# Optimization experiments

Hardware: AMD Instinct MI355X
Metric: run time of the kernel (lower is better)

Reference implementation:

```python
import jax, jax.numpy as jnp
import numpy as np

GROUPSIZE = 4      # g: multivariate group size (d = groupsize - 2)
NB_GROUPS = 48     # f: number of expert groups / filters
CHANNELS = 128     # c: signal channels fed to the L operator
SCALE = 0.999
SLOPE = 1.0        # model_params['scaling']
LAMB_INIT = 0.1
EPS_OMEGA_INIT = -2.0


def proj_l1(x):
    """Euclidean projection onto the unit l1 ball along axis 1. x: [B,G,F,H,W]."""
    ax = jnp.abs(x)
    s = -jnp.sort(-ax, axis=1)                      # descending |x|
    cssv = jnp.cumsum(s, axis=1) - 1.0
    G = x.shape[1]
    k = jnp.arange(1, G + 1, dtype=x.dtype).reshape(1, G, 1, 1, 1)
    cond = s * k > cssv
    rho = jnp.sum(cond, axis=1, keepdims=True)       # number of active coords
    theta = jnp.take_along_axis(cssv, rho - 1, axis=1) / rho.astype(x.dtype)
    theta = jnp.maximum(theta, 0.0)
    proj = jnp.sign(x) * jnp.maximum(ax - theta, 0.0)
    inside = jnp.sum(ax, axis=1, keepdims=True) <= 1.0
    return jnp.where(inside, x, proj)


def _forward(x_noisy, sigma, Q_param, taus_param, lamb, eps_omega,
             mu_w1, mu_b1, mu_w2, mu_b2, mu_w3, mu_b3, Wf, n_iter):
    lamb_e = jnp.exp(lamb)
    eps_e = jnp.exp(eps_omega)

    # --- Q normalization + spectral norms (cached once per forward) ---
    Q = Q_param / jnp.maximum(jnp.sum(jnp.abs(Q_param), axis=2, keepdims=True), 1.0)
    Q_norms = jnp.linalg.svd(Q, compute_uv=False)[:, 0].reshape(-1, 1, 1)  # [F,1,1]
    Q_eff = Q / Q_norms ** 2
    taus = jnp.exp(jax.nn.relu(taus_param))          # [1,1,F,1,1]

    # --- per-batch noise-adaptive scaling via small MLP ---
    h = jax.nn.relu((sigma * 20.0 - 2.0) @ mu_w1 + mu_b1)
    h = jax.nn.relu(h @ mu_w2 + mu_b2)
    h = h @ mu_w3 + mu_b3                            # [B,F]
    scaling = jax.nn.relu(h * 0.05 + sigma) * SLOPE + 1e-9
    scaling = scaling.reshape(-1, 1, scaling.shape[-1], 1, 1)  # [B,1,F,1,1]

    def moreau(x):
        g = proj_l1(x)
        cost = jnp.max(jnp.abs(x - g), axis=1) + 0.5 * jnp.sum(g * g, axis=1)
        cost = cost[:, None]                         # [B,1,F,H,W]
        g = g + eps_e * x
        cost = cost + eps_e * 0.5 * jnp.sqrt(jnp.sum(x * x, axis=1, keepdims=True))
        return g, cost

    def activation(x):
        gc, cc = moreau(x)
        # orient: scale * einsum('flg,bgfhw->blfhw', Q/Q_norms^2, x), then /taus
        y = SCALE * jnp.einsum('flg,bgfhw->blfhw', Q_eff, x) / taus
        gcc, ccc = moreau(y)
        # unorient: scale * einsum with Q^T  (Q^T[f,l,g] = Q[f,g,l])
        gcc = SCALE * jnp.einsum('fgl,bgfhw->blfhw', Q, gcc)
        ccc = Q_norms ** 2 * (taus * ccc)
        return lamb_e * (gc - gcc), lamb_e * (cc - ccc)

    def reconstruct(x):
        Lx = jnp.einsum('gfc,bchw->bgfhw', Wf, x) / scaling
        g, cost = activation(Lx)
        g = jnp.einsum('gfc,bgfhw->bchw', Wf, g * scaling)   # adjoint L^T
        cost = jnp.sum(cost * scaling ** 2, axis=(1, 2, 3, 4))
        g = (x - x_noisy + g) / (1.0 + lamb_e * (1.0 + eps_e))
        cost = cost + 0.5 * jnp.sum((x - x_noisy) ** 2, axis=(1, 2, 3))
        return g, cost

    def step(x, _):
        g, _c = reconstruct(x)
        return x - g, None

    x_final, _ = jax.lax.scan(jax.checkpoint(step), x_noisy, jnp.arange(n_iter))
    return x_final


def setup_inputs() -> dict:
    key = jax.random.key(0)
    ks = jax.random.split(key, 8)
    B, C, H, W = 2, CHANNELS, 128, 128
    F_, G = NB_GROUPS, GROUPSIZE
    x_noisy = jax.random.normal(ks[0], (B, C, H, W), jnp.float32)
    sigma = jax.random.uniform(ks[1], (B, 1), jnp.float32)
    Q_param = jax.random.uniform(ks[2], (F_, G, G), jnp.float32) - 0.5
    taus_param = (LAMB_INIT / 2.0) * jnp.ones((1, 1, F_, 1, 1), jnp.float32)
    lamb = jnp.float32(LAMB_INIT)
    eps_omega = jnp.float32(EPS_OMEGA_INIT)
    mu_w1 = jax.random.normal(ks[3], (1, F_), jnp.float32)
    mu_b1 = jnp.zeros((F_,), jnp.float32)
    mu_w2 = jax.random.normal(ks[4], (F_, F_), jnp.float32) / np.float32(np.sqrt(F_))
    mu_b2 = jnp.zeros((F_,), jnp.float32)
    mu_w3 = jax.random.normal(ks[5], (F_, F_), jnp.float32) / np.float32(np.sqrt(F_))
    mu_b3 = jnp.zeros((F_,), jnp.float32)
    Wf = jax.random.normal(ks[6], (G, F_, C), jnp.float32) / np.float32(np.sqrt(C))
    return dict(x_noisy=x_noisy, sigma=sigma, Q_param=Q_param, taus_param=taus_param,
                lamb=lamb, eps_omega=eps_omega, mu_w1=mu_w1, mu_b1=mu_b1,
                mu_w2=mu_w2, mu_b2=mu_b2, mu_w3=mu_w3, mu_b3=mu_b3, Wf=Wf, n_iter=10)


def reference(x_noisy, sigma, Q_param, taus_param, lamb, eps_omega,
              mu_w1, mu_b1, mu_w2, mu_b2, mu_w3, mu_b3, Wf, n_iter):
    return _forward(x_noisy, sigma, Q_param, taus_param, lamb, eps_omega,
                    mu_w1, mu_b1, mu_w2, mu_b2, mu_w3, mu_b3, Wf, n_iter)
```

## Files before the change

### kernel.cpp

```cpp
#include <hip/hip_runtime.h>
#include <math.h>

#define F_ 48
#define C_ 128
#define HW 16384
#define SCALE_C 0.999f
#define TPB 256
#define MTPB 512

typedef __attribute__((ext_vector_type(4))) float floatx4;
typedef __attribute__((ext_vector_type(8))) _Float16 half8;
typedef __attribute__((ext_vector_type(4))) _Float16 half4;

#define P1_U 0
#define P2_U 49152
#define QEQN_F 49152
#define MISC_F (QEQN_F + 1536)
#define SINV_F (MISC_F + 2)
#define SLAM_F (SINV_F + 96)

__global__ void setup_math(const float* __restrict__ sigma,
                           const float* __restrict__ Qp,
                           const float* __restrict__ taus_p,
                           const float* __restrict__ lamb,
                           const float* __restrict__ eps_om,
                           const float* __restrict__ mw1, const float* __restrict__ mb1,
                           const float* __restrict__ mw2, const float* __restrict__ mb2,
                           const float* __restrict__ mw3, const float* __restrict__ mb3,
                           float* __restrict__ wsf)
{
    const int tid = threadIdx.x;
    if (tid < F_) {
        const int f = tid;
        float Qm[4][4];
        for (int g = 0; g < 4; ++g) {
            float s = 0.f;
            for (int l = 0; l < 4; ++l) s += fabsf(Qp[f * 16 + g * 4 + l]);
            float d = fmaxf(s, 1.0f);
            for (int l = 0; l < 4; ++l) Qm[g][l] = Qp[f * 16 + g * 4 + l] / d;
        }
        double A[4][4];
        for (int i = 0; i < 4; ++i)
            for (int j = 0; j < 4; ++j) {
                double s = 0.0;
                for (int g = 0; g < 4; ++g) s += (double)Qm[g][i] * (double)Qm[g][j];
                A[i][j] = s;
            }
        double M[4][4];
        for (int i = 0; i < 4; ++i) for (int j = 0; j < 4; ++j) M[i][j] = A[i][j];
        for (int it = 0; it < 30; ++it) {
            double T[4][4]; double mx = 0.0;
            for (int i = 0; i < 4; ++i)
                for (int j = 0; j < 4; ++j) {
                    double s = 0.0;
                    for (int k = 0; k < 4; ++k) s += M[i][k] * M[k][j];
                    T[i][j] = s;
                    double a = fabs(s); if (a > mx) mx = a;
                }
            if (mx < 1e-300) break;
            double inv = 1.0 / mx;
            for (int i = 0; i < 4; ++i) for (int j = 0; j < 4; ++j) M[i][j] = T[i][j] * inv;
        }
        int jb = 0; double bn = -1.0;
        for (int j = 0; j < 4; ++j) {
            double nn = 0.0;
            for (int i = 0; i < 4; ++i) nn += M[i][j] * M[i][j];
            if (nn > bn) { bn = nn; jb = j; }
        }
        double v[4]; for (int i = 0; i < 4; ++i) v[i] = M[i][jb];
        double Av[4];
        for (int i = 0; i < 4; ++i) {
            double s = 0.0;
            for (int j = 0; j < 4; ++j) s += A[i][j] * v[j];
            Av[i] = s;
        }
        double vv = 0.0, vav = 0.0;
        for (int i = 0; i < 4; ++i) { vv += v[i] * v[i]; vav += v[i] * Av[i]; }
        float lamf = (float)((vv > 0.0) ? (vav / vv) : 0.0);
        float tau = expf(fmaxf(taus_p[f], 0.0f));
        float qsv = SCALE_C / tau;
        for (int l = 0; l < 4; ++l)
            for (int g = 0; g < 4; ++g)
                wsf[QEQN_F + f * 32 + l * 4 + g] = qsv * Qm[l][g] / lamf;
        for (int g = 0; g < 4; ++g)
            for (int l = 0; l < 4; ++l)
                wsf[QEQN_F + f * 32 + 16 + g * 4 + l] = SCALE_C * Qm[g][l];
    }
    if (tid >= 48 && tid < 50) {
        const int b = tid - 48;
        float lamb_e = expf(lamb[0]);
        float sg = sigma[b];
        float t = sg * 20.0f - 2.0f;
        float h1[F_], h2[F_];
        for (int j = 0; j < F_; ++j) h1[j] = fmaxf(t * mw1[j] + mb1[j], 0.0f);
        for (int j = 0; j < F_; ++j) {
            float s = mb2[j];
            for (int k = 0; k < F_; ++k) s += h1[k] * mw2[k * F_ + j];
            h2[j] = fmaxf(s, 0.0f);
        }
        for (int j = 0; j < F_; ++j) {
            float s = mb3[j];
            for (int k = 0; k < F_; ++k) s += h2[k] * mw3[k * F_ + j];
            float sc = fmaxf(s * 0.05f + sg, 0.0f) + 1e-9f;
            wsf[SINV_F + b * F_ + j] = 1.0f / sc;
            wsf[SLAM_F + b * F_ + j] = lamb_e * sc;
        }
    }
    if (tid == 50) {
        float lamb_e = expf(lamb[0]);
        float eps_e = expf(eps_om[0]);
        wsf[MISC_F + 0] = eps_e;
        wsf[MISC_F + 1] = 1.0f / (1.0f + lamb_e * (1.0f + eps_e));
    }
}

__global__ void setup_pack(const float* __restrict__ Wf, float* __restrict__ wsf)
{
    unsigned short* wsu = (unsigned short*)wsf;
    const int gtid = blockIdx.x * TPB + threadIdx.x;
    for (int i = gtid; i < 98304; i += gridDim.x * TPB) {
        if (i < 49152) {
            int j = i & 7, lane = (i >> 3) & 63;
            int t = i >> 9;
            int ks = t & 3, mtile = t >> 2;
            int rt = lane & 15, qq = lane >> 4;
            int c = ks * 32 + qq * 8 + j;
            int ft = mtile >> 1;
            int f = ft * 4 + (rt >> 2);
            int gl = rt & 3;
            float w;
            if ((mtile & 1) == 0) {
                w = Wf[(gl * F_ + f) * C_ + c];
            } else {
                w = 0.f;
                for (int g = 0; g < 4; ++g)
                    w += wsf[QEQN_F + f * 32 + gl * 4 + g] * Wf[(g * F_ + f) * C_ + c];
            }
            _Float16 hv = (_Float16)w;
            wsu[P1_U + ((mtile * 4 + ks) * 64 + lane) * 8 + j] = *(unsigned short*)&hv;
        } else {
            int ii = i - 49152;
            int j = ii & 7, lane = (ii >> 3) & 63;
            int t = ii >> 9;
            int ks = t % 12, cmt = t / 12;
            int m = lane & 15, qq = lane >> 4;
            int cch = cmt * 16 + m;
            int r = ks * 32 + qq * 8 + j;
            float w;
            if (ks < 6) {
                int f = r >> 2, g = r & 3;
                w = Wf[(g * F_ + f) * C_ + cch];
            } else {
                int rp = r - 192;
                int f = rp >> 2, l = rp & 3;
                w = 0.f;
                for (int g = 0; g < 4; ++g)
                    w += wsf[QEQN_F + f * 32 + 16 + l * 4 + g] * Wf[(g * F_ + f) * C_ + cch];
                w = -w;
            }
            _Float16 hv = (_Float16)w;
            wsu[P2_U + ((cmt * 12 + ks) * 64 + lane) * 8 + j] = *(unsigned short*)&hv;
        }
    }
}

__device__ __forceinline__ void proj4(const float v[4], float o[4]) {
    float a0 = fabsf(v[0]), a1 = fabsf(v[1]), a2 = fabsf(v[2]), a3 = fabsf(v[3]);
    float sum = a0 + a1 + a2 + a3;
    float t0 = fmaxf(a0, a1), u0 = fminf(a0, a1);
    float t1 = fmaxf(a2, a3), u1 = fminf(a2, a3);
    float s0 = fmaxf(t0, t1), m0 = fminf(t0, t1);
    float m1 = fmaxf(u0, u1), s3 = fminf(u0, u1);
    float s1 = fmaxf(m1, m0), s2 = fminf(m1, m0);
    float c2 = s0 + s1, c3 = c2 + s2, c4 = c3 + s3;
    float th = s0 - 1.0f, rs = 1.0f;
    if (s1 * 2.0f > c2 - 1.0f) { th = c2 - 1.0f; rs = 0.5f; }
    if (s2 * 3.0f > c3 - 1.0f) { th = c3 - 1.0f; rs = (1.0f / 3.0f); }
    if (s3 * 4.0f > c4 - 1.0f) { th = c4 - 1.0f; rs = 0.25f; }
    float theta = fmaxf(th * rs, 0.0f);
    bool inside = (sum <= 1.0f);
#pragma unroll
    for (int g = 0; g < 4; ++g) {
        float ag = fabsf(v[g]);
        float pg = copysignf(fmaxf(ag - theta, 0.0f), v[g]);
        o[g] = inside ? v[g] : pg;
    }
}

__global__ __launch_bounds__(MTPB, 4) void mfoe_main(
    const float* __restrict__ xnoisy,
    const float* __restrict__ wsf,
    float* __restrict__ out,
    const int* __restrict__ n_iter_p)
{
    __shared__ __align__(16) _Float16 sXF[4096];
    __shared__ __align__(16) _Float16 sACT[12288];
    __shared__ __align__(16) float sISL[96];

    const int tid = threadIdx.x;
    const int lane = tid & 63;
    const int wv = __builtin_amdgcn_readfirstlane(tid >> 6);
    const int n = lane & 15;
    const int q = lane >> 4;
    const int blk = blockIdx.x;
    const int b = blk >> 9;
    const int pix0 = (blk & 511) << 5;

    const float* __restrict__ xin = xnoisy + b * (C_ * HW) + pix0;
    float* __restrict__ oimg = out + b * (C_ * HW) + pix0;
    const unsigned short* __restrict__ wsu = (const unsigned short*)wsf;
    const int niter = *n_iter_p;

    if (niter == 0) {
        for (int i = tid; i < C_ * 32; i += MTPB) {
            int p = i & 31, c = i >> 5;
            oimg[c * HW + p] = xin[c * HW + p];
        }
        return;
    }

    for (int i = tid; i < C_ * 32; i += MTPB) {
        int p = i & 31, c = i >> 5;
        int idx = ((p >> 4) * 4 + (c >> 5)) * 512 + (((c >> 3) & 3) * 16 + (p & 15)) * 8 + (c & 7);
        sXF[idx] = (_Float16)xin[c * HW + p];
    }
    for (int i = tid; i < 96; i += MTPB) {
        if (i < 48) sISL[i] = wsf[SINV_F + b * F_ + i];
        else        sISL[i] = wsf[SLAM_F + b * F_ + (i - 48)];
    }

    float xnr[8];
#pragma unroll
    for (int j = 0; j < 2; ++j) {
        int jw = wv * 2 + j, cmt = jw >> 1, nt = jw & 1;
        int p = nt * 16 + n;
#pragma unroll
        for (int reg = 0; reg < 4; ++reg)
            xnr[j * 4 + reg] = xin[(cmt * 16 + q * 4 + reg) * HW + p];
    }
    const float eps_e = wsf[MISC_F + 0];
    const float invden = wsf[MISC_F + 1];

    for (int it = 0; it < niter; ++it) {
        __syncthreads();
#pragma unroll 1
        for (int j = 0; j < 3; ++j) {
            int jw = wv * 3 + j, ft = jw >> 1, nt = jw & 1;
            floatx4 accv = (floatx4){0.f, 0.f, 0.f, 0.f};
            floatx4 accy = (floatx4){0.f, 0.f, 0.f, 0.f};
            const half8* aE = (const half8*)(wsu + P1_U + (ft * 8) * 512 + lane * 8);
            const half8* bFp = (const half8*)&sXF[nt * 2048 + lane * 8];
#pragma unroll
            for (int ks = 0; ks < 4; ++ks) {
                half8 bF = bFp[ks * 64];
                accv = __builtin_amdgcn_mfma_f32_16x16x32_f16(aE[ks * 64], bF, accv, 0, 0, 0);
                accy = __builtin_amdgcn_mfma_f32_16x16x32_f16(aE[ks * 64 + 256], bF, accy, 0, 0, 0);
            }
            int f = ft * 4 + q;
            float invs = sISL[f];
            float slam = sISL[48 + f];
            float v[4] = {accv[0] * invs, accv[1] * invs, accv[2] * invs, accv[3] * invs};
            float y[4] = {accy[0] * invs, accy[1] * invs, accy[2] * invs, accy[3] * invs};
            float pv[4]; proj4(v, pv);
            float py[4]; proj4(y, py);
            half4 au, am;
#pragma unroll
            for (int g = 0; g < 4; ++g) {
                au[g] = (_Float16)(fmaf(eps_e, v[g], pv[g]) * slam);
                am[g] = (_Float16)(fmaf(eps_e, y[g], py[g]) * slam);
            }
            int aw = ((nt * 12 + (ft >> 1)) * 64 + ((ft & 1) * 2 + (q >> 1)) * 16 + n) * 8 + (q & 1) * 4;
            *(half4*)&sACT[aw] = au;
            *(half4*)&sACT[aw + 3072] = am;
        }
        __syncthreads();
        floatx4 acc2[2];
#pragma unroll
        for (int j = 0; j < 2; ++j) acc2[j] = (floatx4){0.f, 0.f, 0.f, 0.f};
#pragma unroll
        for (int j = 0; j < 2; ++j) {
            int jw = wv * 2 + j, cmt = jw >> 1, nt = jw & 1;
            const half8* a2F = (const half8*)(wsu + P2_U + (cmt * 12) * 512 + lane * 8);
            const half8* bAp = (const half8*)&sACT[nt * 6144 + lane * 8];
            floatx4 a = acc2[j];
#pragma unroll
            for (int ks = 0; ks < 12; ++ks) {
                half8 aF = a2F[ks * 64];
                half8 bA = bAp[ks * 64];
                a = __builtin_amdgcn_mfma_f32_16x16x32_f16(aF, bA, a, 0, 0, 0);
            }
            acc2[j] = a;
        }
        const bool last = (it == niter - 1);
#pragma unroll
        for (int j = 0; j < 2; ++j) {
            int jw = wv * 2 + j, cmt = jw >> 1, nt = jw & 1;
            int p = nt * 16 + n;
            int cb = cmt * 16 + q * 4;
            int xu = ((nt * 4 + (cmt >> 1)) * 64 + ((cmt & 1) * 2 + (q >> 1)) * 16 + n) * 8 + (q & 1) * 4;
            half4 xo4 = *(const half4*)&sXF[xu];
            float xo0 = (float)xo4[0];
            float xo1 = (float)xo4[1];
            float xo2 = (float)xo4[2];
            float xo3 = (float)xo4[3];
            float nx0 = xo0 - ((xo0 - xnr[j * 4 + 0]) + acc2[j][0]) * invden;
            float nx1 = xo1 - ((xo1 - xnr[j * 4 + 1]) + acc2[j][1]) * invden;
            float nx2 = xo2 - ((xo2 - xnr[j * 4 + 2]) + acc2[j][2]) * invden;
            float nx3 = xo3 - ((xo3 - xnr[j * 4 + 3]) + acc2[j][3]) * invden;
            if (last) {
                oimg[(cb + 0) * HW + p] = nx0;
                oimg[(cb + 1) * HW + p] = nx1;
                oimg[(cb + 2) * HW + p] = nx2;
                oimg[(cb + 3) * HW + p] = nx3;
            }
            half4 nx4;
            nx4[0] = (_Float16)nx0;
            nx4[1] = (_Float16)nx1;
            nx4[2] = (_Float16)nx2;
            nx4[3] = (_Float16)nx3;
            *(half4*)&sXF[xu] = nx4;
        }
    }
}

extern "C" void kernel_launch(void* const* d_in, const int* in_sizes, int n_in,
                              void* d_out, int out_size, void* d_ws, size_t ws_size,
                              hipStream_t stream) {
    const float* x_noisy = (const float*)d_in[0];
    const float* sigma   = (const float*)d_in[1];
    const float* Qp      = (const float*)d_in[2];
    const float* taus_p  = (const float*)d_in[3];
    const float* lamb    = (const float*)d_in[4];
    const float* eps_om  = (const float*)d_in[5];
    const float* mw1     = (const float*)d_in[6];
    const float* mb1     = (const float*)d_in[7];
    const float* mw2     = (const float*)d_in[8];
    const float* mb2     = (const float*)d_in[9];
    const float* mw3     = (const float*)d_in[10];
    const float* mb3     = (const float*)d_in[11];
    const float* Wf      = (const float*)d_in[12];
    const int*   n_iter  = (const int*)d_in[13];
    float* out = (float*)d_out;
    float* ws  = (float*)d_ws;

    hipLaunchKernelGGL(setup_math, dim3(1), dim3(64), 0, stream,
                       sigma, Qp, taus_p, lamb, eps_om,
                       mw1, mb1, mw2, mb2, mw3, mb3, ws);
    hipLaunchKernelGGL(setup_pack, dim3(192), dim3(TPB), 0, stream, Wf, ws);
    hipLaunchKernelGGL(mfoe_main, dim3(1024), dim3(MTPB), 0, stream,
                       x_noisy, ws, out, n_iter);
}
```

Before: 287.0 us.

## Double pixel tile per block to reuse weight fragments across four pixel tiles

Each block now handles 64 pixels instead of 32, halving the grid to 512 blocks. Each wave loads an A weight fragment once and reuses it across two pixel tiles in the first GEMM and four in the second, cutting global/L2 weight reads per MFMA. The iterate x is also kept in fp32 registers instead of being re-read from fp16 LDS, which improves precision and removes LDS reads. The cost is double LDS use, higher register pressure, and fewer blocks, which may reduce occupancy or leave CUs underfilled.

Result: no change. 283.7 us (-1.1%).

```diff
diff --git a/kernel.cpp b/kernel.cpp
--- a/kernel.cpp
+++ b/kernel.cpp
@@ -193,8 +193,8 @@
     float* __restrict__ out,
     const int* __restrict__ n_iter_p)
 {
-    __shared__ __align__(16) _Float16 sXF[4096];
-    __shared__ __align__(16) _Float16 sACT[12288];
+    __shared__ __align__(16) _Float16 sXF[8192];
+    __shared__ __align__(16) _Float16 sACT[24576];
     __shared__ __align__(16) float sISL[96];
 
     const int tid = threadIdx.x;
@@ -203,8 +203,8 @@
     const int n = lane & 15;
     const int q = lane >> 4;
     const int blk = blockIdx.x;
-    const int b = blk >> 9;
-    const int pix0 = (blk & 511) << 5;
+    const int b = blk >> 8;
+    const int pix0 = (blk & 255) << 6;
 
     const float* __restrict__ xin = xnoisy + b * (C_ * HW) + pix0;
     float* __restrict__ oimg = out + b * (C_ * HW) + pix0;
@@ -212,16 +212,16 @@
     const int niter = *n_iter_p;
 
     if (niter == 0) {
-        for (int i = tid; i < C_ * 32; i += MTPB) {
-            int p = i & 31, c = i >> 5;
+        for (int i = tid; i < C_ * 64; i += MTPB) {
+            int p = i & 63, c = i >> 6;
             oimg[c * HW + p] = xin[c * HW + p];
         }
         return;
     }
 
-    for (int i = tid; i < C_ * 32; i += MTPB) {
-        int p = i & 31, c = i >> 5;
-        int idx = ((p >> 4) * 4 + (c >> 5)) * 512 + (((c >> 3) & 3) * 16 + (p & 15)) * 8 + (c & 7);
+    for (int i = tid; i < C_ * 64; i += MTPB) {
+        int p = i & 63, c = i >> 6;
+        int idx = (((p >> 4) * 4 + (c >> 5)) * 64 + ((c >> 3) & 3) * 16 + (p & 15)) * 8 + (c & 7);
         sXF[idx] = (_Float16)xin[c * HW + p];
     }
     for (int i = tid; i < 96; i += MTPB) {
@@ -229,95 +229,96 @@
         else        sISL[i] = wsf[SLAM_F + b * F_ + (i - 48)];
     }
 
-    float xnr[8];
-#pragma unroll
-    for (int j = 0; j < 2; ++j) {
-        int jw = wv * 2 + j, cmt = jw >> 1, nt = jw & 1;
-        int p = nt * 16 + n;
-#pragma unroll
-        for (int reg = 0; reg < 4; ++reg)
-            xnr[j * 4 + reg] = xin[(cmt * 16 + q * 4 + reg) * HW + p];
-    }
+    float xnr[16], xr[16];
+#pragma unroll
+    for (int np = 0; np < 4; ++np)
+#pragma unroll
+        for (int l = 0; l < 4; ++l) {
+            float v = xin[(wv * 16 + q * 4 + l) * HW + np * 16 + n];
+            xnr[np * 4 + l] = v;
+            xr[np * 4 + l] = v;
+        }
     const float eps_e = wsf[MISC_F + 0];
     const float invden = wsf[MISC_F + 1];
 
     for (int it = 0; it < niter; ++it) {
         __syncthreads();
 #pragma unroll 1
-        for (int j = 0; j < 3; ++j) {
-            int jw = wv * 3 + j, ft = jw >> 1, nt = jw & 1;
-            floatx4 accv = (floatx4){0.f, 0.f, 0.f, 0.f};
-            floatx4 accy = (floatx4){0.f, 0.f, 0.f, 0.f};
+        for (int jj = 0; jj < 3; ++jj) {
+            int grp = wv * 3 + jj, ft = grp >> 1, nph = grp & 1;
+            int np0 = nph * 2;
+            floatx4 accv0 = (floatx4){0.f, 0.f, 0.f, 0.f};
+            floatx4 accv1 = (floatx4){0.f, 0.f, 0.f, 0.f};
+            floatx4 accy0 = (floatx4){0.f, 0.f, 0.f, 0.f};
+            floatx4 accy1 = (floatx4){0.f, 0.f, 0.f, 0.f};
             const half8* aE = (const half8*)(wsu + P1_U + (ft * 8) * 512 + lane * 8);
-            const half8* bFp = (const half8*)&sXF[nt * 2048 + lane * 8];
+            const half8* b0 = (const half8*)&sXF[(np0 * 4) * 512 + lane * 8];
+            const half8* b1 = (const half8*)&sXF[((np0 + 1) * 4) * 512 + lane * 8];
 #pragma unroll
             for (int ks = 0; ks < 4; ++ks) {
-                half8 bF = bFp[ks * 64];
-                accv = __builtin_amdgcn_mfma_f32_16x16x32_f16(aE[ks * 64], bF, accv, 0, 0, 0);
-                accy = __builtin_amdgcn_mfma_f32_16x16x32_f16(aE[ks * 64 + 256], bF, accy, 0, 0, 0);
+                half8 aV = aE[ks * 64];
+                half8 aY = aE[ks * 64 + 256];
+                half8 bF0 = b0[ks * 64];
+                half8 bF1 = b1[ks * 64];
+                accv0 = __builtin_amdgcn_mfma_f32_16x16x32_f16(aV, bF0, accv0, 0, 0, 0);
+                accy0 = __builtin_amdgcn_mfma_f32_16x16x32_f16(aY, bF0, accy0, 0, 0, 0);
+                accv1 = __builtin_amdgcn_mfma_f32_16x16x32_f16(aV, bF1, accv1, 0, 0, 0);
+                accy1 = __builtin_amdgcn_mfma_f32_16x16x32_f16(aY, bF1, accy1, 0, 0, 0);
             }
             int f = ft * 4 + q;
             float invs = sISL[f];
             float slam = sISL[48 + f];
-            float v[4] = {accv[0] * invs, accv[1] * invs, accv[2] * invs, accv[3] * invs};
-            float y[4] = {accy[0] * invs, accy[1] * invs, accy[2] * invs, accy[3] * invs};
-            float pv[4]; proj4(v, pv);
-            float py[4]; proj4(y, py);
-            half4 au, am;
-#pragma unroll
-            for (int g = 0; g < 4; ++g) {
-                au[g] = (_Float16)(fmaf(eps_e, v[g], pv[g]) * slam);
-                am[g] = (_Float16)(fmaf(eps_e, y[g], py[g]) * slam);
-            }
-            int aw = ((nt * 12 + (ft >> 1)) * 64 + ((ft & 1) * 2 + (q >> 1)) * 16 + n) * 8 + (q & 1) * 4;
-            *(half4*)&sACT[aw] = au;
-            *(half4*)&sACT[aw + 3072] = am;
+#pragma unroll
+            for (int h = 0; h < 2; ++h) {
+                int np = np0 + h;
+                floatx4 accv = h ? accv1 : accv0;
+                floatx4 accy = h ? accy1 : accy0;
+                float v[4] = {accv[0] * invs, accv[1] * invs, accv[2] * invs, accv[3] * invs};
+                float y[4] = {accy[0] * invs, accy[1] * invs, accy[2] * invs, accy[3] * invs};
+                float pv[4]; proj4(v, pv);
+                float py[4]; proj4(y, py);
+                half4 au, am;
+#pragma unroll
+                for (int g = 0; g < 4; ++g) {
+                    au[g] = (_Float16)(fmaf(eps_e, v[g], pv[g]) * slam);
+                    am[g] = (_Float16)(fmaf(eps_e, y[g], py[g]) * slam);
+                }
+                int aw = ((np * 12 + (ft >> 1)) * 64 + ((ft & 1) * 2 + (q >> 1)) * 16 + n) * 8 + (q & 1) * 4;
+                *(half4*)&sACT[aw] = au;
+                *(half4*)&sACT[aw + 3072] = am;
+            }
         }
         __syncthreads();
-        floatx4 acc2[2];
-#pragma unroll
-        for (int j = 0; j < 2; ++j) acc2[j] = (floatx4){0.f, 0.f, 0.f, 0.f};
-#pragma unroll
-        for (int j = 0; j < 2; ++j) {
-            int jw = wv * 2 + j, cmt = jw >> 1, nt = jw & 1;
-            const half8* a2F = (const half8*)(wsu + P2_U + (cmt * 12) * 512 + lane * 8);
-            const half8* bAp = (const half8*)&sACT[nt * 6144 + lane * 8];
-            floatx4 a = acc2[j];
+        floatx4 acc2[4];
+#pragma unroll
+        for (int np = 0; np < 4; ++np) acc2[np] = (floatx4){0.f, 0.f, 0.f, 0.f};
+        {
+            const half8* a2F = (const half8*)(wsu + P2_U + (wv * 12) * 512 + lane * 8);
+            const half8* bAp = (const half8*)&sACT[lane * 8];
 #pragma unroll
             for (int ks = 0; ks < 12; ++ks) {
                 half8 aF = a2F[ks * 64];
-                half8 bA = bAp[ks * 64];
-                a = __builtin_amdgcn_mfma_f32_16x16x32_f16(aF, bA, a, 0, 0, 0);
-            }
-            acc2[j] = a;
+#pragma unroll
+                for (int np = 0; np < 4; ++np) {
+                    half8 bA = bAp[(np * 12 + ks) * 64];
+                    acc2[np] = __builtin_amdgcn_mfma_f32_16x16x32_f16(aF, bA, acc2[np], 0, 0, 0);
+                }
+            }
         }
         const bool last = (it == niter - 1);
 #pragma unroll
-        for (int j = 0; j < 2; ++j) {
-            int jw = wv * 2 + j, cmt = jw >> 1, nt = jw & 1;
-            int p = nt * 16 + n;
-            int cb = cmt * 16 + q * 4;
-            int xu = ((nt * 4 + (cmt >> 1)) * 64 + ((cmt & 1) * 2 + (q >> 1)) * 16 + n) * 8 + (q & 1) * 4;
-            half4 xo4 = *(const half4*)&sXF[xu];
-            float xo0 = (float)xo4[0];
-            float xo1 = (float)xo4[1];
-            float xo2 = (float)xo4[2];
-            float xo3 = (float)xo4[3];
-            float nx0 = xo0 - ((xo0 - xnr[j * 4 + 0]) + acc2[j][0]) * invden;
-            float nx1 = xo1 - ((xo1 - xnr[j * 4 + 1]) + acc2[j][1]) * invden;
-            float nx2 = xo2 - ((xo2 - xnr[j * 4 + 2]) + acc2[j][2]) * invden;
-            float nx3 = xo3 - ((xo3 - xnr[j * 4 + 3]) + acc2[j][3]) * invden;
-            if (last) {
-                oimg[(cb + 0) * HW + p] = nx0;
-                oimg[(cb + 1) * HW + p] = nx1;
-                oimg[(cb + 2) * HW + p] = nx2;
-                oimg[(cb + 3) * HW + p] = nx3;
-            }
+        for (int np = 0; np < 4; ++np) {
+            int p = np * 16 + n;
             half4 nx4;
-            nx4[0] = (_Float16)nx0;
-            nx4[1] = (_Float16)nx1;
-            nx4[2] = (_Float16)nx2;
-            nx4[3] = (_Float16)nx3;
+#pragma unroll
+            for (int l = 0; l < 4; ++l) {
+                float xo = xr[np * 4 + l];
+                float nx = xo - ((xo - xnr[np * 4 + l]) + acc2[np][l]) * invden;
+                xr[np * 4 + l] = nx;
+                nx4[l] = (_Float16)nx;
+                if (last) oimg[(wv * 16 + q * 4 + l) * HW + p] = nx;
+            }
+            int xu = ((np * 4 + (wv >> 1)) * 64 + ((wv & 1) * 2 + (q >> 1)) * 16 + n) * 8 + (q & 1) * 4;
             *(half4*)&sXF[xu] = nx4;
         }
     }
@@ -347,6 +348,6 @@
                        sigma, Qp, taus_p, lamb, eps_om,
                        mw1, mb1, mw2, mb2, mw3, mb3, ws);
     hipLaunchKernelGGL(setup_pack, dim3(192), dim3(TPB), 0, stream, Wf, ws);
-    hipLaunchKernelGGL(mfoe_main, dim3(1024), dim3(MTPB), 0, stream,
+    hipLaunchKernelGGL(mfoe_main, dim3(512), dim3(MTPB), 0, stream,
                        x_noisy, ws, out, n_iter);
 }
```

## Fold Q-transpose orientation into activation epilogue, halving second GEMM K dimension

Applied to the files above, without the earlier changes.

The second GEMM previously ran over a stacked K of 384 (plain Wf rows plus a Q-premultiplied copy). This change applies the 4x4 Q mix per pixel in registers during the activation epilogue, so the GEMM now uses only the 192-wide Wf operand and a single activation buffer. The l1 projection is also rewritten as a branchless max over candidate thresholds, with the eps term fused in. Shared activation memory and packed weights are halved, in exchange for 16 extra FMAs and a small shared-memory Q table read per group. The branchless theta and the dropped inside-ball case must stay numerically equivalent to the original.

Result: faster. 273.6 us (-4.6%).

```diff
diff --git a/kernel.cpp b/kernel.cpp
--- a/kernel.cpp
+++ b/kernel.cpp
@@ -14,7 +14,7 @@
 
 #define P1_U 0
 #define P2_U 49152
-#define QEQN_F 49152
+#define QEQN_F 36864
 #define MISC_F (QEQN_F + 1536)
 #define SINV_F (MISC_F + 2)
 #define SLAM_F (SINV_F + 96)
@@ -118,7 +118,7 @@
 {
     unsigned short* wsu = (unsigned short*)wsf;
     const int gtid = blockIdx.x * TPB + threadIdx.x;
-    for (int i = gtid; i < 98304; i += gridDim.x * TPB) {
+    for (int i = gtid; i < 73728; i += gridDim.x * TPB) {
         if (i < 49152) {
             int j = i & 7, lane = (i >> 3) & 63;
             int t = i >> 9;
@@ -142,48 +142,38 @@
             int ii = i - 49152;
             int j = ii & 7, lane = (ii >> 3) & 63;
             int t = ii >> 9;
-            int ks = t % 12, cmt = t / 12;
+            int ks = t % 6, cmt = t / 6;
             int m = lane & 15, qq = lane >> 4;
             int cch = cmt * 16 + m;
             int r = ks * 32 + qq * 8 + j;
-            float w;
-            if (ks < 6) {
-                int f = r >> 2, g = r & 3;
-                w = Wf[(g * F_ + f) * C_ + cch];
-            } else {
-                int rp = r - 192;
-                int f = rp >> 2, l = rp & 3;
-                w = 0.f;
-                for (int g = 0; g < 4; ++g)
-                    w += wsf[QEQN_F + f * 32 + 16 + l * 4 + g] * Wf[(g * F_ + f) * C_ + cch];
-                w = -w;
-            }
+            int f = r >> 2, g = r & 3;
+            float w = Wf[(g * F_ + f) * C_ + cch];
             _Float16 hv = (_Float16)w;
-            wsu[P2_U + ((cmt * 12 + ks) * 64 + lane) * 8 + j] = *(unsigned short*)&hv;
-        }
-    }
-}
-
-__device__ __forceinline__ void proj4(const float v[4], float o[4]) {
+            wsu[P2_U + ((cmt * 6 + ks) * 64 + lane) * 8 + j] = *(unsigned short*)&hv;
+        }
+    }
+}
+
+__device__ __forceinline__ void actmerge(const float v[4], float eps, float o[4]) {
     float a0 = fabsf(v[0]), a1 = fabsf(v[1]), a2 = fabsf(v[2]), a3 = fabsf(v[3]);
-    float sum = a0 + a1 + a2 + a3;
-    float t0 = fmaxf(a0, a1), u0 = fminf(a0, a1);
-    float t1 = fmaxf(a2, a3), u1 = fminf(a2, a3);
-    float s0 = fmaxf(t0, t1), m0 = fminf(t0, t1);
-    float m1 = fmaxf(u0, u1), s3 = fminf(u0, u1);
-    float s1 = fmaxf(m1, m0), s2 = fminf(m1, m0);
-    float c2 = s0 + s1, c3 = c2 + s2, c4 = c3 + s3;
-    float th = s0 - 1.0f, rs = 1.0f;
-    if (s1 * 2.0f > c2 - 1.0f) { th = c2 - 1.0f; rs = 0.5f; }
-    if (s2 * 3.0f > c3 - 1.0f) { th = c3 - 1.0f; rs = (1.0f / 3.0f); }
-    if (s3 * 4.0f > c4 - 1.0f) { th = c4 - 1.0f; rs = 0.25f; }
-    float theta = fmaxf(th * rs, 0.0f);
-    bool inside = (sum <= 1.0f);
+    float lo01 = fminf(a0, a1), hi01 = fmaxf(a0, a1);
+    float lo23 = fminf(a2, a3), hi23 = fmaxf(a2, a3);
+    float c4 = (a0 + a1) + (a2 + a3);
+    float mn1 = fminf(lo01, lo23);
+    float mn2 = fminf(fmaxf(lo01, lo23), fminf(hi01, hi23));
+    float c1 = fmaxf(hi01, hi23);
+    float c3 = c4 - mn1;
+    float c2 = c3 - mn2;
+    float t1 = c1 - 1.0f;
+    float t2 = (c2 - 1.0f) * 0.5f;
+    float t3 = (c3 - 1.0f) * (1.0f / 3.0f);
+    float t4 = (c4 - 1.0f) * 0.25f;
+    float theta = fmaxf(fmaxf(fmaxf(t1, t2), fmaxf(t3, t4)), 0.0f);
+    float aa[4] = {a0, a1, a2, a3};
 #pragma unroll
     for (int g = 0; g < 4; ++g) {
-        float ag = fabsf(v[g]);
-        float pg = copysignf(fmaxf(ag - theta, 0.0f), v[g]);
-        o[g] = inside ? v[g] : pg;
+        float r = fmaf(eps, aa[g], fmaxf(aa[g] - theta, 0.0f));
+        o[g] = copysignf(r, v[g]);
     }
 }
 
@@ -194,7 +184,8 @@
     const int* __restrict__ n_iter_p)
 {
     __shared__ __align__(16) _Float16 sXF[4096];
-    __shared__ __align__(16) _Float16 sACT[12288];
+    __shared__ __align__(16) _Float16 sACT[6144];
+    __shared__ __align__(16) float sQS[F_ * 16];
     __shared__ __align__(16) float sISL[96];
 
     const int tid = threadIdx.x;
@@ -224,6 +215,8 @@
         int idx = ((p >> 4) * 4 + (c >> 5)) * 512 + (((c >> 3) & 3) * 16 + (p & 15)) * 8 + (c & 7);
         sXF[idx] = (_Float16)xin[c * HW + p];
     }
+    for (int i = tid; i < F_ * 16; i += MTPB)
+        sQS[i] = wsf[QEQN_F + (i >> 4) * 32 + 16 + (i & 15)];
     for (int i = tid; i < 96; i += MTPB) {
         if (i < 48) sISL[i] = wsf[SINV_F + b * F_ + i];
         else        sISL[i] = wsf[SLAM_F + b * F_ + (i - 48)];
@@ -231,93 +224,89 @@
 
     float xnr[8];
 #pragma unroll
-    for (int j = 0; j < 2; ++j) {
-        int jw = wv * 2 + j, cmt = jw >> 1, nt = jw & 1;
-        int p = nt * 16 + n;
-#pragma unroll
-        for (int reg = 0; reg < 4; ++reg)
-            xnr[j * 4 + reg] = xin[(cmt * 16 + q * 4 + reg) * HW + p];
-    }
+    for (int nt = 0; nt < 2; ++nt)
+#pragma unroll
+        for (int l = 0; l < 4; ++l)
+            xnr[nt * 4 + l] = xin[(wv * 16 + q * 4 + l) * HW + nt * 16 + n];
+
     const float eps_e = wsf[MISC_F + 0];
     const float invden = wsf[MISC_F + 1];
+
+    const half8* __restrict__ A1 = (const half8*)wsu;
+    const half8* __restrict__ A2 = (const half8*)(wsu + P2_U);
+    const half8* __restrict__ sXF8 = (const half8*)sXF;
+    const half8* __restrict__ sACT8 = (const half8*)sACT;
 
     for (int it = 0; it < niter; ++it) {
         __syncthreads();
 #pragma unroll 1
-        for (int j = 0; j < 3; ++j) {
-            int jw = wv * 3 + j, ft = jw >> 1, nt = jw & 1;
+        for (int jj = 0; jj < 3; ++jj) {
+            const int grp = wv * 3 + jj;
+            const int ft = grp >> 1;
+            const int nt = grp & 1;
             floatx4 accv = (floatx4){0.f, 0.f, 0.f, 0.f};
             floatx4 accy = (floatx4){0.f, 0.f, 0.f, 0.f};
-            const half8* aE = (const half8*)(wsu + P1_U + (ft * 8) * 512 + lane * 8);
-            const half8* bFp = (const half8*)&sXF[nt * 2048 + lane * 8];
 #pragma unroll
             for (int ks = 0; ks < 4; ++ks) {
-                half8 bF = bFp[ks * 64];
-                accv = __builtin_amdgcn_mfma_f32_16x16x32_f16(aE[ks * 64], bF, accv, 0, 0, 0);
-                accy = __builtin_amdgcn_mfma_f32_16x16x32_f16(aE[ks * 64 + 256], bF, accy, 0, 0, 0);
+                half8 aV = A1[((ft * 2 + 0) * 4 + ks) * 64 + lane];
+                half8 aY = A1[((ft * 2 + 1) * 4 + ks) * 64 + lane];
+                half8 bF = sXF8[(nt * 4 + ks) * 64 + lane];
+                accv = __builtin_amdgcn_mfma_f32_16x16x32_f16(aV, bF, accv, 0, 0, 0);
+                accy = __builtin_amdgcn_mfma_f32_16x16x32_f16(aY, bF, accy, 0, 0, 0);
             }
-            int f = ft * 4 + q;
-            float invs = sISL[f];
-            float slam = sISL[48 + f];
+            const int f = ft * 4 + q;
+            const float invs = sISL[f];
+            const float slam = sISL[48 + f];
+            float qs[16];
+#pragma unroll
+            for (int k = 0; k < 4; ++k)
+                *(floatx4*)&qs[4 * k] = *(const floatx4*)&sQS[f * 16 + 4 * k];
             float v[4] = {accv[0] * invs, accv[1] * invs, accv[2] * invs, accv[3] * invs};
             float y[4] = {accy[0] * invs, accy[1] * invs, accy[2] * invs, accy[3] * invs};
-            float pv[4]; proj4(v, pv);
-            float py[4]; proj4(y, py);
-            half4 au, am;
-#pragma unroll
-            for (int g = 0; g < 4; ++g) {
-                au[g] = (_Float16)(fmaf(eps_e, v[g], pv[g]) * slam);
-                am[g] = (_Float16)(fmaf(eps_e, y[g], py[g]) * slam);
+            float uv[4]; actmerge(v, eps_e, uv);
+            float m2[4]; actmerge(y, eps_e, m2);
+            float a0 = (uv[0] - fmaf(qs[0], m2[0], fmaf(qs[4], m2[1],
+                        fmaf(qs[8], m2[2], qs[12] * m2[3])))) * slam;
+            float a1 = (uv[1] - fmaf(qs[1], m2[0], fmaf(qs[5], m2[1],
+                        fmaf(qs[9], m2[2], qs[13] * m2[3])))) * slam;
+            float a2 = (uv[2] - fmaf(qs[2], m2[0], fmaf(qs[6], m2[1],
+                        fmaf(qs[10], m2[2], qs[14] * m2[3])))) * slam;
+            float a3 = (uv[3] - fmaf(qs[3], m2[0], fmaf(qs[7], m2[1],
+                        fmaf(qs[11], m2[2], qs[15] * m2[3])))) * slam;
+            half4 av4;
+            av4[0] = (_Float16)a0;
+            av4[1] = (_Float16)a1;
+            av4[2] = (_Float16)a2;
+            av4[3] = (_Float16)a3;
+            int aw = ((nt * 6 + (ft >> 1)) * 64 + ((ft & 1) * 2 + (q >> 1)) * 16 + n) * 8 + (q & 1) * 4;
+            *(half4*)&sACT[aw] = av4;
+        }
+        __syncthreads();
+        floatx4 acc20 = (floatx4){0.f, 0.f, 0.f, 0.f};
+        floatx4 acc21 = (floatx4){0.f, 0.f, 0.f, 0.f};
+#pragma unroll
+        for (int ks = 0; ks < 6; ++ks) {
+            half8 aF = A2[(wv * 6 + ks) * 64 + lane];
+            half8 bA0 = sACT8[(0 * 6 + ks) * 64 + lane];
+            half8 bA1 = sACT8[(1 * 6 + ks) * 64 + lane];
+            acc20 = __builtin_amdgcn_mfma_f32_16x16x32_f16(aF, bA0, acc20, 0, 0, 0);
+            acc21 = __builtin_amdgcn_mfma_f32_16x16x32_f16(aF, bA1, acc21, 0, 0, 0);
+        }
+        const bool last = (it == niter - 1);
+#pragma unroll
+        for (int nt = 0; nt < 2; ++nt) {
+            floatx4 acc = nt ? acc21 : acc20;
+            int p = nt * 16 + n;
+            int xu = ((nt * 4 + (wv >> 1)) * 64 + ((wv & 1) * 2 + (q >> 1)) * 16 + n) * 8 + (q & 1) * 4;
+            half4 xo4 = *(const half4*)&sXF[xu];
+            half4 nx4;
+#pragma unroll
+            for (int l = 0; l < 4; ++l) {
+                float xo = (float)xo4[l];
+                float nx = xo - ((xo - xnr[nt * 4 + l]) + acc[l]) * invden;
+                nx4[l] = (_Float16)nx;
+                if (last) oimg[(wv * 16 + q * 4 + l) * HW + p] = nx;
             }
-            int aw = ((nt * 12 + (ft >> 1)) * 64 + ((ft & 1) * 2 + (q >> 1)) * 16 + n) * 8 + (q & 1) * 4;
-            *(half4*)&sACT[aw] = au;
-            *(half4*)&sACT[aw + 3072] = am;
-        }
-        __syncthreads();
-        floatx4 acc2[2];
-#pragma unroll
-        for (int j = 0; j < 2; ++j) acc2[j] = (floatx4){0.f, 0.f, 0.f, 0.f};
-#pragma unroll
-        for (int j = 0; j < 2; ++j) {
-            int jw = wv * 2 + j, cmt = jw >> 1, nt = jw & 1;
-            const half8* a2F = (const half8*)(wsu + P2_U + (cmt * 12) * 512 + lane * 8);
-            const half8* bAp = (const half8*)&sACT[nt * 6144 + lane * 8];
-            floatx4 a = acc2[j];
-#pragma unroll
-            for (int ks = 0; ks < 12; ++ks) {
-                half8 aF = a2F[ks * 64];
-                half8 bA = bAp[ks * 64];
-                a = __builtin_amdgcn_mfma_f32_16x16x32_f16(aF, bA, a, 0, 0, 0);
-            }
-            acc2[j] = a;
-        }
-        const bool last = (it == niter - 1);
-#pragma unroll
-        for (int j = 0; j < 2; ++j) {
-            int jw = wv * 2 + j, cmt = jw >> 1, nt = jw & 1;
-            int p = nt * 16 + n;
-            int cb = cmt * 16 + q * 4;
-            int xu = ((nt * 4 + (cmt >> 1)) * 64 + ((cmt & 1) * 2 + (q >> 1)) * 16 + n) * 8 + (q & 1) * 4;
-            half4 xo4 = *(const half4*)&sXF[xu];
-            float xo0 = (float)xo4[0];
-            float xo1 = (float)xo4[1];
-            float xo2 = (float)xo4[2];
-            float xo3 = (float)xo4[3];
-            float nx0 = xo0 - ((xo0 - xnr[j * 4 + 0]) + acc2[j][0]) * invden;
-            float nx1 = xo1 - ((xo1 - xnr[j * 4 + 1]) + acc2[j][1]) * invden;
-            float nx2 = xo2 - ((xo2 - xnr[j * 4 + 2]) + acc2[j][2]) * invden;
-            float nx3 = xo3 - ((xo3 - xnr[j * 4 + 3]) + acc2[j][3]) * invden;
-            if (last) {
-                oimg[(cb + 0) * HW + p] = nx0;
-                oimg[(cb + 1) * HW + p] = nx1;
-                oimg[(cb + 2) * HW + p] = nx2;
-                oimg[(cb + 3) * HW + p] = nx3;
-            }
-            half4 nx4;
-            nx4[0] = (_Float16)nx0;
-            nx4[1] = (_Float16)nx1;
-            nx4[2] = (_Float16)nx2;
-            nx4[3] = (_Float16)nx3;
             *(half4*)&sXF[xu] = nx4;
         }
     }
```
